# Kernel tuning notes

Hardware: AMD Instinct MI355X
Metric: run time of the kernel (lower is better)

## Reference

```python
import jax, jax.numpy as jnp
import numpy as np

V, E, H = 50257, 512, 1024  # vocab, embed_dim, hidden_dim
B, S = 64, 2048             # batch, src_len


def setup_inputs() -> dict:
    key = jax.random.key(0)
    ks = jax.random.split(key, 16)
    sc = 0.02
    emb = jax.random.normal(ks[0], (V, E), jnp.float32) * sc
    emb = emb.at[0].set(0.0)  # padding_idx=0
    return {
        "x": jax.random.randint(ks[1], (B, 1), 0, V),
        "hidden": jax.random.normal(ks[2], (1, B, H), jnp.float32),
        "cell": jax.random.normal(ks[3], (1, B, H), jnp.float32),
        "encoder_outputs": jax.random.normal(ks[4], (B, S, H), jnp.float32),
        "emb": emb,
        "Wa_w": jax.random.normal(ks[5], (H, H), jnp.float32) * sc,
        "Wa_b": jnp.zeros((H,), jnp.float32),
        "Ua_w": jax.random.normal(ks[6], (H, H), jnp.float32) * sc,
        "Ua_b": jnp.zeros((H,), jnp.float32),
        "va_w": jax.random.normal(ks[7], (1, H), jnp.float32) * sc,
        "va_b": jnp.zeros((1,), jnp.float32),
        "Wih": jax.random.normal(ks[8], (4 * H, E + H), jnp.float32) * sc,
        "Whh": jax.random.normal(ks[9], (4 * H, H), jnp.float32) * sc,
        "bih": jnp.zeros((4 * H,), jnp.float32),
        "bhh": jnp.zeros((4 * H,), jnp.float32),
        "fc_w": jax.random.normal(ks[10], (V, H), jnp.float32) * sc,
        "fc_b": jnp.zeros((V,), jnp.float32),
    }


def reference(x, hidden, cell, encoder_outputs, emb, Wa_w, Wa_b, Ua_w, Ua_b,
              va_w, va_b, Wih, Whh, bih, bhh, fc_w, fc_b):
    # Embedding lookup: [B,1] -> [B,E]
    embedded = emb[x[:, 0]]
    # Bahdanau additive attention
    s_t = hidden[-1]                                          # [B,H]
    proj_s = jnp.einsum('bh,oh->bo', s_t, Wa_w) + Wa_b        # [B,H]
    proj_e = jnp.einsum('bsh,oh->bso', encoder_outputs, Ua_w) + Ua_b  # [B,S,H]
    e = jnp.tanh(proj_s[:, None, :] + proj_e)                 # [B,S,H]
    scores = jnp.einsum('bsh,h->bs', e, va_w[0]) + va_b[0]    # [B,S]
    attn = jax.nn.softmax(scores, axis=1)                     # [B,S]
    context = jnp.einsum('bs,bsh->bh', attn, encoder_outputs)  # [B,H]
    # Single-step LSTM (torch gate order: i, f, g, o)
    lstm_in = jnp.concatenate([embedded, context], axis=1)    # [B,E+H]
    gates = lstm_in @ Wih.T + bih + s_t @ Whh.T + bhh         # [B,4H]
    i, f, g, o = jnp.split(gates, 4, axis=1)
    i, f, o = jax.nn.sigmoid(i), jax.nn.sigmoid(f), jax.nn.sigmoid(o)
    g = jnp.tanh(g)
    c_new = f * cell[-1] + i * g
    h_new = o * jnp.tanh(c_new)
    predictions = (h_new @ fc_w.T + fc_b)[:, None, :]          # [B,1,V]
    return predictions, h_new[None], c_new[None]
```

## Files before the change

kernel.cpp:

```cpp
#include <hip/hip_runtime.h>
#include <hip/hip_bf16.h>

#define V_ 50257
#define H_ 1024
#define S_ 2048

typedef float f32x4 __attribute__((ext_vector_type(4)));
typedef short s16x8 __attribute__((ext_vector_type(8)));

__device__ __forceinline__ unsigned short f2bf(float f){
  unsigned u = __builtin_bit_cast(unsigned, f);
  return (unsigned short)((u + 0x7FFFu + ((u >> 16) & 1u)) >> 16);
}
__device__ __forceinline__ unsigned cvt2(float a, float b){
  return (unsigned)f2bf(a) | ((unsigned)f2bf(b) << 16);
}
__device__ __forceinline__ float bf2f(unsigned short h){
  return __builtin_bit_cast(float, (unsigned)h << 16);
}
__device__ __forceinline__ float fast_tanh(float x){
  return 1.0f - 2.0f/(__expf(2.0f*x)+1.0f);
}
__device__ __forceinline__ float fast_sig(float x){
  return 1.0f/(1.0f+__expf(-x));
}
__device__ __forceinline__ void gld_lds16(const void* g, void* l){
  __builtin_amdgcn_global_load_lds((const __attribute__((address_space(1))) void*)g,
                                   (__attribute__((address_space(3))) void*)l, 16, 0, 0);
}

__global__ __launch_bounds__(256) void k_cvt_bf16(const float* __restrict__ src,
                                                  unsigned short* __restrict__ dst, int n){
  int i = (blockIdx.x*256 + threadIdx.x)*4;
  if (i < n){
    float4 f = *(const float4*)(src + i);
    uint2 u;
    u.x = cvt2(f.x, f.y);
    u.y = cvt2(f.z, f.w);
    *(uint2*)(dst + i) = u;
  }
}

__global__ __launch_bounds__(256) void k_cvt_enc(const float* __restrict__ src,
                                                 unsigned short* __restrict__ dst){
  const size_t stride = (size_t)gridDim.x * 256;
  const float4* s4 = (const float4*)src;
  uint2* d2 = (uint2*)dst;
  for (size_t i = (size_t)blockIdx.x*256 + threadIdx.x; i < 33554432u; i += stride){
    float4 f = s4[i];
    uint2 u;
    u.x = cvt2(f.x, f.y);
    u.y = cvt2(f.z, f.w);
    d2[i] = u;
  }
}

__global__ __launch_bounds__(256) void k_proje_bf(
    const unsigned short* __restrict__ A,
    const unsigned short* __restrict__ Bw,
    const float* __restrict__ ps,
    const float* __restrict__ Ua_b,
    const float* __restrict__ va,
    float* __restrict__ part)
{
  __shared__ unsigned short Al[128*64];
  __shared__ unsigned short Bl[128*64];
  const int t = threadIdx.x;
  const int lane = t & 63, wid = t >> 6;
  const int lr = lane & 15, lk = lane >> 4;
  int bid = blockIdx.x;
  int L = (bid & 7) * 1024 + (bid >> 3);
  const int wgm = L >> 3, wgn = L & 7;
  const int m0 = wgm * 128, n0 = wgn * 128;
  const int wm = wid >> 1, wn = wid & 1;

  const int srow = lane >> 3;
  const int schunk = (lane & 7) ^ srow;
  const unsigned short* aBase = A + (size_t)(m0 + wid*32 + srow)*1024 + schunk*8;
  const unsigned short* bBase = Bw + (size_t)(n0 + wid*32 + srow)*1024 + schunk*8;

  f32x4 acc[4][4] = {};

  for (int kt = 0; kt < 16; ++kt){
    __syncthreads();
    #pragma unroll
    for (int i = 0; i < 4; ++i){
      gld_lds16(aBase + kt*64 + i*8*1024, Al + (wid*32 + i*8)*64);
      gld_lds16(bBase + kt*64 + i*8*1024, Bl + (wid*32 + i*8)*64);
    }
    __syncthreads();
    #pragma unroll
    for (int ks = 0; ks < 2; ++ks){
      s16x8 af[4], bfr[4];
      #pragma unroll
      for (int mi = 0; mi < 4; ++mi){
        int r = wm*64 + mi*16 + lr;
        af[mi] = *(const s16x8*)(Al + r*64 + (((ks*4+lk) ^ (lr&7))*8));
      }
      #pragma unroll
      for (int ni = 0; ni < 4; ++ni){
        int r = wn*64 + ni*16 + lr;
        bfr[ni] = *(const s16x8*)(Bl + r*64 + (((ks*4+lk) ^ (lr&7))*8));
      }
      #pragma unroll
      for (int mi = 0; mi < 4; ++mi)
        #pragma unroll
        for (int ni = 0; ni < 4; ++ni)
          acc[mi][ni] = __builtin_amdgcn_mfma_f32_16x16x32_bf16(af[mi], bfr[ni], acc[mi][ni], 0,0,0);
    }
  }
  const int b = m0 >> 11;
  float psv[4], vav[4];
  #pragma unroll
  for (int ni = 0; ni < 4; ++ni){
    int n = n0 + wn*64 + ni*16 + lr;
    psv[ni] = ps[b*1024 + n] + Ua_b[n];
    vav[ni] = va[n];
  }
  #pragma unroll
  for (int mi = 0; mi < 4; ++mi){
    float p0=0.f,p1=0.f,p2=0.f,p3=0.f;
    #pragma unroll
    for (int ni = 0; ni < 4; ++ni){
      p0 += vav[ni]*fast_tanh(acc[mi][ni][0] + psv[ni]);
      p1 += vav[ni]*fast_tanh(acc[mi][ni][1] + psv[ni]);
      p2 += vav[ni]*fast_tanh(acc[mi][ni][2] + psv[ni]);
      p3 += vav[ni]*fast_tanh(acc[mi][ni][3] + psv[ni]);
    }
    #pragma unroll
    for (int off = 1; off < 16; off <<= 1){
      p0 += __shfl_xor(p0, off);
      p1 += __shfl_xor(p1, off);
      p2 += __shfl_xor(p2, off);
      p3 += __shfl_xor(p3, off);
    }
    if (lr == 0){
      int rg = m0 + wm*64 + mi*16 + lk*4;
      int slot = wgn*2 + wn;
      part[(size_t)rg*16 + slot]     = p0;
      part[(size_t)(rg+1)*16 + slot] = p1;
      part[(size_t)(rg+2)*16 + slot] = p2;
      part[(size_t)(rg+3)*16 + slot] = p3;
    }
  }
}

__global__ __launch_bounds__(256,2) void k_proje_f32(
    const float* __restrict__ A,
    const unsigned short* __restrict__ Bw,
    const float* __restrict__ ps,
    const float* __restrict__ Ua_b,
    const float* __restrict__ va,
    float* __restrict__ part)
{
  __shared__ unsigned char sm[32768];
  const int t = threadIdx.x;
  const int lane = t & 63, wid = t >> 6;
  const int lr = lane & 15, lk = lane >> 4;
  int bid = blockIdx.x;
  int L = (bid & 7) * 1024 + (bid >> 3);
  const int wgm = L >> 3, wgn = L & 7;
  const int m0 = wgm * 128, n0 = wgn * 128;
  const int wm = wid >> 1, wn = wid & 1;

  f32x4 acc[4][4] = {};
  const int row2 = t >> 1, half = t & 1;
  const float* aSrc = A + (size_t)(m0 + row2) * 1024 + half * 32;
  const unsigned short* bSrc = Bw + (size_t)(n0 + row2) * 1024 + half * 32;
  unsigned char* Al = sm;
  unsigned char* Bl = sm + 16384;
  const int swzr = row2 & 7;

  for (int kt = 0; kt < 16; ++kt){
    __syncthreads();
    #pragma unroll
    for (int c = 0; c < 4; ++c){
      float4 f0 = *(const float4*)(aSrc + kt*64 + c*8);
      float4 f1 = *(const float4*)(aSrc + kt*64 + c*8 + 4);
      union { unsigned u[4]; s16x8 v; } p;
      p.u[0]=cvt2(f0.x,f0.y); p.u[1]=cvt2(f0.z,f0.w);
      p.u[2]=cvt2(f1.x,f1.y); p.u[3]=cvt2(f1.z,f1.w);
      int ch = half*4 + c;
      *(s16x8*)(Al + row2*128 + ((ch ^ swzr)*16)) = p.v;
    }
    #pragma unroll
    for (int c = 0; c < 4; ++c){
      s16x8 v = *(const s16x8*)(bSrc + kt*64 + (half*4 + c)*8);
      *(s16x8*)(Bl + row2*128 + (((half*4+c) ^ swzr)*16)) = v;
    }
    __syncthreads();
    #pragma unroll
    for (int ks = 0; ks < 2; ++ks){
      s16x8 af[4], bfr[4];
      #pragma unroll
      for (int mi = 0; mi < 4; ++mi){
        int r = wm*64 + mi*16 + lr;
        af[mi] = *(const s16x8*)(Al + r*128 + (((ks*4+lk) ^ (lr&7))*16));
      }
      #pragma unroll
      for (int ni = 0; ni < 4; ++ni){
        int r = wn*64 + ni*16 + lr;
        bfr[ni] = *(const s16x8*)(Bl + r*128 + (((ks*4+lk) ^ (lr&7))*16));
      }
      #pragma unroll
      for (int mi = 0; mi < 4; ++mi)
        #pragma unroll
        for (int ni = 0; ni < 4; ++ni)
          acc[mi][ni] = __builtin_amdgcn_mfma_f32_16x16x32_bf16(af[mi], bfr[ni], acc[mi][ni], 0,0,0);
    }
  }
  const int b = m0 >> 11;
  float psv[4], vav[4];
  #pragma unroll
  for (int ni = 0; ni < 4; ++ni){
    int n = n0 + wn*64 + ni*16 + lr;
    psv[ni] = ps[b*1024 + n] + Ua_b[n];
    vav[ni] = va[n];
  }
  #pragma unroll
  for (int mi = 0; mi < 4; ++mi){
    float p0=0.f,p1=0.f,p2=0.f,p3=0.f;
    #pragma unroll
    for (int ni = 0; ni < 4; ++ni){
      p0 += vav[ni]*fast_tanh(acc[mi][ni][0] + psv[ni]);
      p1 += vav[ni]*fast_tanh(acc[mi][ni][1] + psv[ni]);
      p2 += vav[ni]*fast_tanh(acc[mi][ni][2] + psv[ni]);
      p3 += vav[ni]*fast_tanh(acc[mi][ni][3] + psv[ni]);
    }
    #pragma unroll
    for (int off = 1; off < 16; off <<= 1){
      p0 += __shfl_xor(p0, off);
      p1 += __shfl_xor(p1, off);
      p2 += __shfl_xor(p2, off);
      p3 += __shfl_xor(p3, off);
    }
    if (lr == 0){
      int rg = m0 + wm*64 + mi*16 + lk*4;
      int slot = wgn*2 + wn;
      part[(size_t)rg*16 + slot]     = p0;
      part[(size_t)(rg+1)*16 + slot] = p1;
      part[(size_t)(rg+2)*16 + slot] = p2;
      part[(size_t)(rg+3)*16 + slot] = p3;
    }
  }
}

__global__ __launch_bounds__(256,2) void k_gemm64(
    const float* __restrict__ A,
    const float* __restrict__ B1,
    const float* __restrict__ B2,
    const float* __restrict__ bias1,
    const float* __restrict__ bias2,
    float* __restrict__ C, int ldC,
    int N, int K, int K1)
{
  __shared__ unsigned char sm[16384];
  const int t = threadIdx.x;
  const int lane = t & 63, wid = t >> 6;
  const int lr = lane & 15, lk = lane >> 4;
  const int n0 = blockIdx.x * 64;
  f32x4 acc[4] = {};
  const int row = t >> 2, seg = t & 3;
  unsigned char* Al = sm;
  unsigned char* Bl = sm + 8192;
  const int swzr = row & 7;
  const int K2 = K - K1;

  for (int k0 = 0; k0 < K; k0 += 64){
    __syncthreads();
    {
      const float* s = A + (size_t)row*K + k0 + seg*16;
      #pragma unroll
      for (int c = 0; c < 2; ++c){
        float4 f0 = *(const float4*)(s + c*8);
        float4 f1 = *(const float4*)(s + c*8 + 4);
        union { unsigned u[4]; s16x8 v; } p;
        p.u[0]=cvt2(f0.x,f0.y); p.u[1]=cvt2(f0.z,f0.w);
        p.u[2]=cvt2(f1.x,f1.y); p.u[3]=cvt2(f1.z,f1.w);
        *(s16x8*)(Al + row*128 + (((seg*2+c) ^ swzr)*16)) = p.v;
      }
    }
    {
      int n = n0 + row;
      #pragma unroll
      for (int c = 0; c < 2; ++c){
        union { unsigned u[4]; s16x8 v; } p;
        if (n < N){
          int k = k0 + seg*16 + c*8;
          const float* s;
          if (k < K1) s = B1 + (size_t)n*K1 + k;
          else        s = B2 + (size_t)n*K2 + (k - K1);
          float4 f0 = *(const float4*)(s);
          float4 f1 = *(const float4*)(s + 4);
          p.u[0]=cvt2(f0.x,f0.y); p.u[1]=cvt2(f0.z,f0.w);
          p.u[2]=cvt2(f1.x,f1.y); p.u[3]=cvt2(f1.z,f1.w);
        } else {
          p.u[0]=0u; p.u[1]=0u; p.u[2]=0u; p.u[3]=0u;
        }
        *(s16x8*)(Bl + row*128 + (((seg*2+c) ^ swzr)*16)) = p.v;
      }
    }
    __syncthreads();
    #pragma unroll
    for (int ks = 0; ks < 2; ++ks){
      s16x8 bfr = *(const s16x8*)(Bl + (wid*16+lr)*128 + (((ks*4+lk) ^ (lr&7))*16));
      #pragma unroll
      for (int mi = 0; mi < 4; ++mi){
        s16x8 af = *(const s16x8*)(Al + (mi*16+lr)*128 + (((ks*4+lk) ^ (lr&7))*16));
        acc[mi] = __builtin_amdgcn_mfma_f32_16x16x32_bf16(af, bfr, acc[mi], 0,0,0);
      }
    }
  }
  int n = n0 + wid*16 + lr;
  if (n < N){
    float bv = (bias1 ? bias1[n] : 0.f) + (bias2 ? bias2[n] : 0.f);
    #pragma unroll
    for (int mi = 0; mi < 4; ++mi){
      #pragma unroll
      for (int r = 0; r < 4; ++r){
        C[(size_t)(mi*16 + lk*4 + r)*ldC + n] = acc[mi][r] + bv;
      }
    }
  }
}

__global__ __launch_bounds__(256) void k_softmax(const float* __restrict__ part,
                                                 const float* __restrict__ va_b,
                                                 float* __restrict__ attn){
  __shared__ float sc[2048];
  __shared__ float red[8];
  const int b = blockIdx.x, t = threadIdx.x;
  float vb = va_b[0];
  float lmax = -1e30f;
  #pragma unroll
  for (int j = 0; j < 8; ++j){
    int s = t + j*256;
    const float* p = part + ((size_t)b*2048 + s)*16;
    float v = vb;
    #pragma unroll
    for (int i = 0; i < 16; ++i) v += p[i];
    sc[s] = v;
    lmax = fmaxf(lmax, v);
  }
  for (int off = 32; off; off >>= 1) lmax = fmaxf(lmax, __shfl_xor(lmax, off));
  if ((t&63)==0) red[t>>6] = lmax;
  __syncthreads();
  float m = fmaxf(fmaxf(red[0],red[1]),fmaxf(red[2],red[3]));
  float lsum = 0.f;
  #pragma unroll
  for (int j = 0; j < 8; ++j){
    int s = t + j*256;
    float e = __expf(sc[s]-m);
    sc[s] = e; lsum += e;
  }
  for (int off = 32; off; off >>= 1) lsum += __shfl_xor(lsum, off);
  if ((t&63)==0) red[4 + (t>>6)] = lsum;
  __syncthreads();
  float inv = 1.f/(red[4]+red[5]+red[6]+red[7]);
  #pragma unroll
  for (int j = 0; j < 8; ++j){
    int s = t + j*256;
    attn[(size_t)b*2048+s] = sc[s]*inv;
  }
}

__global__ __launch_bounds__(256) void k_context_bf(const float* __restrict__ attn,
                                                    const unsigned short* __restrict__ encb,
                                                    float* __restrict__ ctxp){
  const int b = blockIdx.x >> 3, scid = blockIdx.x & 7;
  const int t = threadIdx.x;
  float a0=0.f,a1=0.f,a2=0.f,a3=0.f;
  const unsigned short* e = encb + ((size_t)b*2048 + scid*256)*1024 + t*4;
  const float* at = attn + (size_t)b*2048 + scid*256;
  #pragma unroll 4
  for (int s = 0; s < 256; ++s){
    float a = at[s];
    ushort4 v = *(const ushort4*)(e + (size_t)s*1024);
    a0 += a*bf2f(v.x); a1 += a*bf2f(v.y); a2 += a*bf2f(v.z); a3 += a*bf2f(v.w);
  }
  float4 o; o.x=a0; o.y=a1; o.z=a2; o.w=a3;
  *(float4*)(ctxp + ((size_t)scid*64 + b)*1024 + t*4) = o;
}

__global__ __launch_bounds__(256) void k_context_f32(const float* __restrict__ attn,
                                                     const float* __restrict__ enc,
                                                     float* __restrict__ ctxp){
  const int b = blockIdx.x >> 3, scid = blockIdx.x & 7;
  const int t = threadIdx.x;
  float a0=0.f,a1=0.f,a2=0.f,a3=0.f;
  const float* e = enc + ((size_t)b*2048 + scid*256)*1024;
  const float* at = attn + (size_t)b*2048 + scid*256;
  for (int s = 0; s < 256; ++s){
    float a = at[s];
    const float* er = e + (size_t)s*1024;
    a0 += a*er[t]; a1 += a*er[t+256]; a2 += a*er[t+512]; a3 += a*er[t+768];
  }
  float* o = ctxp + ((size_t)scid*64 + b)*1024;
  o[t]=a0; o[t+256]=a1; o[t+512]=a2; o[t+768]=a3;
}

__global__ __launch_bounds__(256) void k_build(const int* __restrict__ x,
                                               const float* __restrict__ emb,
                                               const float* __restrict__ ctxp,
                                               const float* __restrict__ hidden,
                                               float* __restrict__ lstm){
  const int b = blockIdx.x, t = threadIdx.x;
  int xe = x[b];
  for (int col = t; col < 2560; col += 256){
    float v;
    if (col < 512) v = emb[(size_t)xe*512 + col];
    else if (col < 1536){
      int h = col - 512;
      v = 0.f;
      #pragma unroll
      for (int i = 0; i < 8; ++i) v += ctxp[((size_t)i*64 + b)*1024 + h];
    } else v = hidden[(size_t)b*1024 + (col-1536)];
    lstm[(size_t)b*2560 + col] = v;
  }
}

__global__ __launch_bounds__(256) void k_lstm(const float* __restrict__ gates,
                                              const float* __restrict__ cell,
                                              float* __restrict__ out){
  int idx = blockIdx.x*256 + threadIdx.x;
  int b = idx >> 10, h = idx & 1023;
  const float* g = gates + (size_t)b*4096;
  float gi = fast_sig(g[h]);
  float gf = fast_sig(g[h+1024]);
  float gg = fast_tanh(g[h+2048]);
  float go = fast_sig(g[h+3072]);
  float c  = gf*cell[idx] + gi*gg;
  float hn = go*fast_tanh(c);
  out[(size_t)V_*64 + idx]         = hn;
  out[(size_t)V_*64 + 65536 + idx] = c;
}

extern "C" void kernel_launch(void* const* d_in, const int* in_sizes, int n_in,
                              void* d_out, int out_size, void* d_ws, size_t ws_size,
                              hipStream_t stream){
  const int*   x     = (const int*)d_in[0];
  const float* hidden= (const float*)d_in[1];
  const float* cell  = (const float*)d_in[2];
  const float* enc   = (const float*)d_in[3];
  const float* emb   = (const float*)d_in[4];
  const float* Wa_w  = (const float*)d_in[5];
  const float* Wa_b  = (const float*)d_in[6];
  const float* Ua_w  = (const float*)d_in[7];
  const float* Ua_b  = (const float*)d_in[8];
  const float* va_w  = (const float*)d_in[9];
  const float* va_b  = (const float*)d_in[10];
  const float* Wih   = (const float*)d_in[11];
  const float* Whh   = (const float*)d_in[12];
  const float* bih   = (const float*)d_in[13];
  const float* bhh   = (const float*)d_in[14];
  const float* fc_w  = (const float*)d_in[15];
  const float* fc_b  = (const float*)d_in[16];
  float* out = (float*)d_out;
  char* ws = (char*)d_ws;
  unsigned short* ua_bf = (unsigned short*)(ws + 0);
  float* ps    = (float*)(ws + 2097152);
  float* attn  = (float*)(ws + 2359296);
  float* lstm  = (float*)(ws + 2883584);
  float* gates = (float*)(ws + 3538944);
  float* ctxp  = (float*)(ws + 4587520);
  float* part  = (float*)(ws + 6684672);
  unsigned short* enc_bf = (unsigned short*)(ws + 16777216);
  const size_t REQ = 16777216u + 268435456u;

  hipLaunchKernelGGL(k_cvt_bf16, dim3(1024), dim3(256), 0, stream, Ua_w, ua_bf, 1048576);
  hipLaunchKernelGGL(k_gemm64, dim3(16), dim3(256), 0, stream,
                     hidden, Wa_w, nullptr, Wa_b, nullptr, ps, 1024, 1024, 1024, 1024);
  if (ws_size >= REQ){
    hipLaunchKernelGGL(k_cvt_enc, dim3(8192), dim3(256), 0, stream, enc, enc_bf);
    hipLaunchKernelGGL(k_proje_bf, dim3(8192), dim3(256), 0, stream,
                       enc_bf, ua_bf, ps, Ua_b, va_w, part);
    hipLaunchKernelGGL(k_softmax, dim3(64), dim3(256), 0, stream, part, va_b, attn);
    hipLaunchKernelGGL(k_context_bf, dim3(512), dim3(256), 0, stream, attn, enc_bf, ctxp);
  } else {
    hipLaunchKernelGGL(k_proje_f32, dim3(8192), dim3(256), 0, stream,
                       enc, ua_bf, ps, Ua_b, va_w, part);
    hipLaunchKernelGGL(k_softmax, dim3(64), dim3(256), 0, stream, part, va_b, attn);
    hipLaunchKernelGGL(k_context_f32, dim3(512), dim3(256), 0, stream, attn, enc, ctxp);
  }
  hipLaunchKernelGGL(k_build, dim3(64), dim3(256), 0, stream, x, emb, ctxp, hidden, lstm);
  hipLaunchKernelGGL(k_gemm64, dim3(64), dim3(256), 0, stream,
                     lstm, Wih, Whh, bih, bhh, gates, 4096, 4096, 2560, 1536);
  hipLaunchKernelGGL(k_lstm, dim3(256), dim3(256), 0, stream, gates, cell, out);
  hipLaunchKernelGGL(k_gemm64, dim3(786), dim3(256), 0, stream,
                     out + (size_t)V_*64, fc_w, nullptr, fc_b, nullptr, out, V_, V_, 1024, 1024);
}
```

Baseline: 709.5 us.

## Enlarge proj_e GEMM tile to 256x256 with double-buffered async LDS staging

Replaces the 128x128, 4-wave attention-projection GEMM with a 256x256 tile run by 8 waves (512 threads), using 128 KB of dynamic LDS split into two buffers. Global-to-LDS loads for the next k-step are issued while the current buffer is consumed, with explicit vmcnt waits and scheduling barriers, plus setprio around the MFMA bursts. The goal is more operand reuse per byte loaded and hiding load latency behind compute. In exchange it runs one block per CU with a heavy register footprint (32 accumulators per lane), so occupancy drops and register spills become possible.

```diff
diff --git a/kernel.cpp b/kernel.cpp
--- a/kernel.cpp
+++ b/kernel.cpp
@@ -28,6 +28,10 @@
   __builtin_amdgcn_global_load_lds((const __attribute__((address_space(1))) void*)g,
                                    (__attribute__((address_space(3))) void*)l, 16, 0, 0);
 }
+
+#define BAR() do { __builtin_amdgcn_sched_barrier(0); __builtin_amdgcn_s_barrier(); __builtin_amdgcn_sched_barrier(0); } while(0)
+#define VMW8() asm volatile("s_waitcnt vmcnt(8)" ::: "memory")
+#define VMW0() asm volatile("s_waitcnt vmcnt(0)" ::: "memory")
 
 __global__ __launch_bounds__(256) void k_cvt_bf16(const float* __restrict__ src,
                                                   unsigned short* __restrict__ dst, int n){
@@ -55,7 +59,7 @@
   }
 }
 
-__global__ __launch_bounds__(256) void k_proje_bf(
+__global__ __launch_bounds__(512,1) void k_proje256(
     const unsigned short* __restrict__ A,
     const unsigned short* __restrict__ Bw,
     const float* __restrict__ ps,
@@ -63,62 +67,103 @@
     const float* __restrict__ va,
     float* __restrict__ part)
 {
-  __shared__ unsigned short Al[128*64];
-  __shared__ unsigned short Bl[128*64];
+  extern __shared__ unsigned short smem[];
   const int t = threadIdx.x;
   const int lane = t & 63, wid = t >> 6;
   const int lr = lane & 15, lk = lane >> 4;
+  const int wr = wid >> 2, wc = wid & 3;
+
   int bid = blockIdx.x;
-  int L = (bid & 7) * 1024 + (bid >> 3);
-  const int wgm = L >> 3, wgn = L & 7;
-  const int m0 = wgm * 128, n0 = wgn * 128;
-  const int wm = wid >> 1, wn = wid & 1;
+  int L = (bid & 7) * 256 + (bid >> 3);
+  const int wgm = L >> 2, wgn = L & 3;
+  const int m0 = wgm * 256, n0 = wgn * 256;
 
   const int srow = lane >> 3;
   const int schunk = (lane & 7) ^ srow;
-  const unsigned short* aBase = A + (size_t)(m0 + wid*32 + srow)*1024 + schunk*8;
-  const unsigned short* bBase = Bw + (size_t)(n0 + wid*32 + srow)*1024 + schunk*8;
-
-  f32x4 acc[4][4] = {};
-
-  for (int kt = 0; kt < 16; ++kt){
-    __syncthreads();
-    #pragma unroll
-    for (int i = 0; i < 4; ++i){
-      gld_lds16(aBase + kt*64 + i*8*1024, Al + (wid*32 + i*8)*64);
-      gld_lds16(bBase + kt*64 + i*8*1024, Bl + (wid*32 + i*8)*64);
-    }
-    __syncthreads();
-    #pragma unroll
-    for (int ks = 0; ks < 2; ++ks){
-      s16x8 af[4], bfr[4];
-      #pragma unroll
-      for (int mi = 0; mi < 4; ++mi){
-        int r = wm*64 + mi*16 + lr;
-        af[mi] = *(const s16x8*)(Al + r*64 + (((ks*4+lk) ^ (lr&7))*8));
-      }
-      #pragma unroll
-      for (int ni = 0; ni < 4; ++ni){
-        int r = wn*64 + ni*16 + lr;
-        bfr[ni] = *(const s16x8*)(Bl + r*64 + (((ks*4+lk) ^ (lr&7))*8));
-      }
-      #pragma unroll
-      for (int mi = 0; mi < 4; ++mi)
-        #pragma unroll
-        for (int ni = 0; ni < 4; ++ni)
-          acc[mi][ni] = __builtin_amdgcn_mfma_f32_16x16x32_bf16(af[mi], bfr[ni], acc[mi][ni], 0,0,0);
-    }
-  }
+
+  f32x4 acc[8][4] = {};
+  s16x8 af[4], bfr[4];
+
+  auto STAGE = [&](int slot, int kt){
+    #pragma unroll
+    for (int h = 0; h < 4; ++h){
+      const unsigned short* gsrc = (h < 2) ? A : Bw;
+      const size_t g0 = (h < 2) ? (size_t)m0 : (size_t)n0;
+      unsigned short* ldst = smem + ((h < 2) ? 0 : 32768) + slot*16384;
+      #pragma unroll
+      for (int j = 0; j < 2; ++j){
+        int rb = (h & 1)*128 + j*64 + wid*8;
+        gld_lds16(gsrc + (g0 + rb + srow)*1024 + kt*64 + schunk*8,
+                  ldst + rb*64);
+      }
+    }
+  };
+
+#define SUBPH(As_, Bs_, msel, ks, LOADB) do { \
+    if (LOADB){ \
+      _Pragma("unroll") \
+      for (int ni = 0; ni < 4; ++ni){ \
+        int rl = wc*64 + ni*16 + lr; \
+        bfr[ni] = *(const s16x8*)((Bs_) + rl*64 + ((((ks)*4+lk) ^ (lr&7))*8)); \
+      } \
+    } \
+    _Pragma("unroll") \
+    for (int mi = 0; mi < 4; ++mi){ \
+      int rl = wr*128 + ((msel)*4+mi)*16 + lr; \
+      af[mi] = *(const s16x8*)((As_) + rl*64 + ((((ks)*4+lk) ^ (lr&7))*8)); \
+    } \
+    __builtin_amdgcn_s_setprio(1); \
+    _Pragma("unroll") \
+    for (int mi = 0; mi < 4; ++mi) \
+      _Pragma("unroll") \
+      for (int ni = 0; ni < 4; ++ni) \
+        acc[(msel)*4+mi][ni] = __builtin_amdgcn_mfma_f32_16x16x32_bf16(af[mi], bfr[ni], acc[(msel)*4+mi][ni], 0,0,0); \
+    __builtin_amdgcn_s_setprio(0); \
+  } while(0)
+
+#define HALF(slot) do { \
+    const unsigned short* As_ = smem + (slot)*16384; \
+    const unsigned short* Bs_ = smem + 32768 + (slot)*16384; \
+    SUBPH(As_, Bs_, 0, 0, 1); \
+    SUBPH(As_, Bs_, 1, 0, 0); \
+    SUBPH(As_, Bs_, 0, 1, 1); \
+    SUBPH(As_, Bs_, 1, 1, 0); \
+  } while(0)
+
+  STAGE(0, 0);
+  STAGE(1, 1);
+  VMW8(); BAR();
+
+  for (int i = 0; i < 8; ++i){
+    HALF(0);
+    if (i < 7){
+      BAR();
+      STAGE(0, 2*i + 2);
+      VMW8();
+      BAR();
+    } else {
+      VMW0();
+      BAR();
+    }
+    HALF(1);
+    if (i < 7){
+      BAR();
+      STAGE(1, 2*i + 3);
+      VMW8();
+      BAR();
+    }
+  }
+
   const int b = m0 >> 11;
   float psv[4], vav[4];
   #pragma unroll
   for (int ni = 0; ni < 4; ++ni){
-    int n = n0 + wn*64 + ni*16 + lr;
+    int n = n0 + wc*64 + ni*16 + lr;
     psv[ni] = ps[b*1024 + n] + Ua_b[n];
     vav[ni] = va[n];
   }
   #pragma unroll
-  for (int mi = 0; mi < 4; ++mi){
+  for (int mi = 0; mi < 8; ++mi){
     float p0=0.f,p1=0.f,p2=0.f,p3=0.f;
     #pragma unroll
     for (int ni = 0; ni < 4; ++ni){
@@ -135,14 +180,16 @@
       p3 += __shfl_xor(p3, off);
     }
     if (lr == 0){
-      int rg = m0 + wm*64 + mi*16 + lk*4;
-      int slot = wgn*2 + wn;
+      int rg = m0 + wr*128 + mi*16 + lk*4;
+      int slot = wgn*4 + wc;
       part[(size_t)rg*16 + slot]     = p0;
       part[(size_t)(rg+1)*16 + slot] = p1;
       part[(size_t)(rg+2)*16 + slot] = p2;
       part[(size_t)(rg+3)*16 + slot] = p3;
     }
   }
+#undef SUBPH
+#undef HALF
 }
 
 __global__ __launch_bounds__(256,2) void k_proje_f32(
@@ -472,7 +519,7 @@
                      hidden, Wa_w, nullptr, Wa_b, nullptr, ps, 1024, 1024, 1024, 1024);
   if (ws_size >= REQ){
     hipLaunchKernelGGL(k_cvt_enc, dim3(8192), dim3(256), 0, stream, enc, enc_bf);
-    hipLaunchKernelGGL(k_proje_bf, dim3(8192), dim3(256), 0, stream,
+    hipLaunchKernelGGL(k_proje256, dim3(2048), dim3(512), 131072, stream,
                        enc_bf, ua_bf, ps, Ua_b, va_w, part);
     hipLaunchKernelGGL(k_softmax, dim3(64), dim3(256), 0, stream, part, va_b, attn);
     hipLaunchKernelGGL(k_context_bf, dim3(512), dim3(256), 0, stream, attn, enc_bf, ctxp);
```

Measured after the change: 698.9 us. About the same (-1.5%).
